# Performance work log

Hardware: AMD Instinct MI355X
Metric: run time of the kernel (lower is better)

Reference implementation:

```python
import jax, jax.numpy as jnp
import numpy as np

STRIDE, PADDING, DILATION, K = 1, 1, 1, 3


def setup_inputs() -> dict:
    key = jax.random.key(0)
    kx, kw, kb = jax.random.split(key, 3)
    x = jax.random.normal(kx, (8, 64, 56, 56), jnp.float32)
    weight = jax.random.normal(kw, (64, 64, K, K), jnp.float32) * 0.05
    bias = jax.random.normal(kb, (64,), jnp.float32)
    # 256x256 LUT of (approximate) int8 products; here the exact product table
    # q_i * q_j for q in [-128, 127], indexed by (q+128).
    q = jnp.arange(256, dtype=jnp.float32) - 128.0
    lut = q[:, None] * q[None, :]
    return {"x": x, "weight": weight, "bias": bias, "lut": lut}


def _quant_int8(t):
    # symmetric per-tensor int8 quantization
    s = jnp.max(jnp.abs(t)) / 127.0
    q = jnp.clip(jnp.round(t / s), -128.0, 127.0).astype(jnp.int32)
    return q, s


def _lut_conv(x, weight, lut):
    B, C, H, W = x.shape
    O = weight.shape[0]
    xq, sx = _quant_int8(x)
    wq, sw = _quant_int8(weight)
    # im2col: patches [B, C*K*K, Ho, Wo]; zero padding quantizes to index 128 (q=0)
    patches = jax.lax.conv_general_dilated_patches(
        xq.astype(jnp.float32), (K, K), (STRIDE, STRIDE),
        [(PADDING, PADDING), (PADDING, PADDING)],
        rhs_dilation=(DILATION, DILATION))
    _, CKK, Ho, Wo = patches.shape
    P = Ho * Wo
    xp = patches.astype(jnp.int32).reshape(B, CKK, P).transpose(0, 2, 1)  # [B,P,CKK]
    wq_flat = wq.reshape(O, CKK)                                          # [O,CKK]
    lut_flat = lut.reshape(-1)                                            # [65536]
    base = (xp + 128) * 256                                               # [B,P,CKK]

    def step(carry, w_o):
        # gather approximate products for one output channel and accumulate
        vals = jnp.take(lut_flat, base + (w_o + 128))  # [B,P,CKK]
        return carry, vals.sum(-1)                     # [B,P]

    _, acc = jax.lax.scan(step, None, wq_flat)         # [O,B,P]
    out = acc.transpose(1, 0, 2).reshape(B, O, Ho, Wo) * (sx * sw)
    return out


def reference(x, weight, bias, lut):
    return _lut_conv(x, weight, lut) + bias[None, :, None, None]
```

## Files before the change

kernel.cpp:

```cpp
#include <hip/hip_runtime.h>


#define BATCH 8
#define CIN   64
#define HH    56
#define WW    56
#define OUTC  64
#define IMG   (HH * WW)
#define TW    58

typedef unsigned int u32;
typedef int v4i __attribute__((ext_vector_type(4)));

__device__ __forceinline__ u32 qpack4(float v0, float v1, float v2, float v3, float s) {
    u32 p = 0;
    float q;
    q = fminf(fmaxf(rintf(v0 / s), -128.0f), 127.0f); p |= ((u32)((int)q & 0xff));
    q = fminf(fmaxf(rintf(v1 / s), -128.0f), 127.0f); p |= ((u32)((int)q & 0xff)) << 8;
    q = fminf(fmaxf(rintf(v2 / s), -128.0f), 127.0f); p |= ((u32)((int)q & 0xff)) << 16;
    q = fminf(fmaxf(rintf(v3 / s), -128.0f), 127.0f); p |= ((u32)((int)q & 0xff)) << 24;
    return p;
}

__global__ __launch_bounds__(256) void max_quantw_kernel(
    const float4* __restrict__ x4, const float4* __restrict__ w4,
    const float* __restrict__ wt,
    float* __restrict__ partsx, u32* __restrict__ wq,
    float* __restrict__ scales) {
    __shared__ float red[4];
    int t = threadIdx.x;
    int blk = blockIdx.x;
    if (blk < 784) {
        int base = blk * 512 + t;
        float4 a = x4[base];
        float4 b = x4[base + 256];
        float m = fmaxf(fmaxf(fmaxf(fabsf(a.x), fabsf(a.y)), fmaxf(fabsf(a.z), fabsf(a.w))),
                        fmaxf(fmaxf(fabsf(b.x), fabsf(b.y)), fmaxf(fabsf(b.z), fabsf(b.w))));
        #pragma unroll
        for (int off = 32; off > 0; off >>= 1)
            m = fmaxf(m, __shfl_down(m, off));
        if ((t & 63) == 0) red[t >> 6] = m;
        __syncthreads();
        if (t == 0)
            partsx[blk] = fmaxf(fmaxf(red[0], red[1]), fmaxf(red[2], red[3]));
    } else {
        float m = 0.0f;
        #pragma unroll 4
        for (int k = 0; k < 36; ++k) {
            float4 a = w4[k * 256 + t];
            m = fmaxf(m, fmaxf(fmaxf(fabsf(a.x), fabsf(a.y)), fmaxf(fabsf(a.z), fabsf(a.w))));
        }
        #pragma unroll
        for (int off = 32; off > 0; off >>= 1)
            m = fmaxf(m, __shfl_down(m, off));
        if ((t & 63) == 0) red[t >> 6] = m;
        __syncthreads();
        float mw = fmaxf(fmaxf(red[0], red[1]), fmaxf(red[2], red[3]));
        float sw = mw / 127.0f;
        if (blk == 784 && t == 0) scales[0] = sw;
        int oc = (blk - 784) * 16 + (t >> 4);
        int cg = t & 15;
        const float4* wb = (const float4*)(wt + oc * 576 + cg * 36);
        float v[36];
        #pragma unroll
        for (int i = 0; i < 9; ++i) {
            float4 f = wb[i];
            v[4 * i + 0] = f.x; v[4 * i + 1] = f.y;
            v[4 * i + 2] = f.z; v[4 * i + 3] = f.w;
        }
        #pragma unroll
        for (int tap = 0; tap < 9; ++tap)
            wq[(oc * 9 + tap) * 16 + cg] =
                qpack4(v[tap], v[9 + tap], v[18 + tap], v[27 + tap], sw);
    }
}

__global__ __launch_bounds__(256) void fused_conv_kernel(
    const float* __restrict__ x, const u32* __restrict__ wq,
    const float* __restrict__ partsx, const float* __restrict__ scales,
    const float* __restrict__ bias, float* __restrict__ out) {
    __shared__ char wl[576 * 80];
    __shared__ char xl[232 * 80];
    __shared__ float sred[4];

    int t = threadIdx.x;
    int lane = t & 63, wid = t >> 6;

    float m = fmaxf(fmaxf(partsx[t], partsx[t + 256]), partsx[t + 512]);
    if (t < 16) m = fmaxf(m, partsx[t + 768]);
    #pragma unroll
    for (int off = 32; off > 0; off >>= 1)
        m = fmaxf(m, __shfl_down(m, off));
    if (lane == 0) sred[wid] = m;
    __syncthreads();
    float mx = fmaxf(fmaxf(sred[0], sred[1]), fmaxf(sred[2], sred[3]));
    float sx = mx / 127.0f;
    float sw = scales[0];

    #pragma unroll
    for (int i = 0; i < 9; ++i) {
        int g = i * 256 + t;
        v4i v = *(const v4i*)((const char*)wq + (size_t)g * 16);
        *(v4i*)(wl + (g >> 2) * 80 + (g & 3) * 16) = v;
    }

    int p0 = blockIdx.x * 64;
    int b = p0 / IMG;
    int hw0 = p0 % IMG;
    int r0 = hw0 / WW;
    #pragma unroll
    for (int iter = 0; iter < 4; ++iter) {
        int item = iter * 256 + t;
        if (item < 928) {
            int s = item >> 2;
            int cg = item & 3;
            int i = s / TW, j2 = s % TW;
            int ro = r0 - 1 + i;
            int co = j2 - 1;
            u32 q0 = 0, q1 = 0, q2 = 0, q3 = 0;
            if (ro >= 0 && ro < HH && co >= 0 && co < WW) {
                const float* xb = x + ((size_t)(b * CIN + cg * 16)) * IMG + ro * WW + co;
                q0 = qpack4(xb[0 * IMG], xb[1 * IMG], xb[2 * IMG], xb[3 * IMG], sx);
                q1 = qpack4(xb[4 * IMG], xb[5 * IMG], xb[6 * IMG], xb[7 * IMG], sx);
                q2 = qpack4(xb[8 * IMG], xb[9 * IMG], xb[10 * IMG], xb[11 * IMG], sx);
                q3 = qpack4(xb[12 * IMG], xb[13 * IMG], xb[14 * IMG], xb[15 * IMG], sx);
            }
            v4i qv = {(int)q0, (int)q1, (int)q2, (int)q3};
            *(v4i*)(xl + s * 80 + cg * 16) = qv;
        }
    }
    __syncthreads();

    int m16 = lane & 15, kq = lane >> 4;
    int prel = wid * 16 + m16;
    int hw = hw0 + prel;
    int h = hw / WW, w = hw % WW;
    const char* abase = xl + ((h - r0) * TW + w) * 80 + kq * 16;
    const char* bbase = wl + m16 * 9 * 80 + kq * 16;

    v4i acc0 = {0, 0, 0, 0}, acc1 = {0, 0, 0, 0};
    v4i acc2 = {0, 0, 0, 0}, acc3 = {0, 0, 0, 0};
    #pragma unroll
    for (int kh = 0; kh < 3; ++kh) {
        #pragma unroll
        for (int kw = 0; kw < 3; ++kw) {
            int tap = kh * 3 + kw;
            v4i av = *(const v4i*)(abase + (kh * TW + kw) * 80);
            v4i b0 = *(const v4i*)(bbase + tap * 80);
            v4i b1 = *(const v4i*)(bbase + tap * 80 + 16 * 9 * 80);
            v4i b2 = *(const v4i*)(bbase + tap * 80 + 32 * 9 * 80);
            v4i b3 = *(const v4i*)(bbase + tap * 80 + 48 * 9 * 80);
            acc0 = __builtin_amdgcn_mfma_i32_16x16x64_i8(av, b0, acc0, 0, 0, 0);
            acc1 = __builtin_amdgcn_mfma_i32_16x16x64_i8(av, b1, acc1, 0, 0, 0);
            acc2 = __builtin_amdgcn_mfma_i32_16x16x64_i8(av, b2, acc2, 0, 0, 0);
            acc3 = __builtin_amdgcn_mfma_i32_16x16x64_i8(av, b3, acc3, 0, 0, 0);
        }
    }

    float scale = sx * sw;
    int pout = hw0 + wid * 16 + kq * 4;
    v4i accs[4] = {acc0, acc1, acc2, acc3};
    #pragma unroll
    for (int tile = 0; tile < 4; ++tile) {
        int oc = tile * 16 + m16;
        float bv = bias[oc];
        float4 r;
        r.x = (float)accs[tile][0] * scale + bv;
        r.y = (float)accs[tile][1] * scale + bv;
        r.z = (float)accs[tile][2] * scale + bv;
        r.w = (float)accs[tile][3] * scale + bv;
        *(float4*)(out + ((size_t)(b * OUTC + oc)) * IMG + pout) = r;
    }
}

extern "C" void kernel_launch(void* const* d_in, const int* in_sizes, int n_in,
                              void* d_out, int out_size, void* d_ws, size_t ws_size,
                              hipStream_t stream) {
    const float* x    = (const float*)d_in[0];
    const float* wt   = (const float*)d_in[1];
    const float* bias = (const float*)d_in[2];

    char* ws = (char*)d_ws;
    float* partsx = (float*)ws;
    float* scales = (float*)(ws + 3200);
    u32*   wq     = (u32*)(ws + 4096);

    max_quantw_kernel<<<788, 256, 0, stream>>>(
        (const float4*)x, (const float4*)wt, wt, partsx, wq, scales);
    fused_conv_kernel<<<392, 256, 0, stream>>>(
        x, wq, partsx, scales, bias, (float*)d_out);
}
```

Before: 85.19 us.

## Split activation quantization into separate kernel writing padded int8 NHWC buffer

Moves int8 quantization of x out of the conv kernel into a dedicated kernel that writes a zero-padded NHWC int8 tensor to workspace, with extra blocks writing the border zeros. The conv kernel then reads MFMA A operands directly from global memory instead of building a halo tile in LDS. This removes the redundant halo quantization, about 3.6x per pixel across 16-channel strided loads, and cuts the fp32 reads. The cost is an extra kernel launch, a global round trip of the int8 activations, and uncoalesced global A loads in the MFMA loop.

```diff
diff --git a/kernel.cpp b/kernel.cpp
--- a/kernel.cpp
+++ b/kernel.cpp
@@ -7,7 +7,8 @@
 #define WW    56
 #define OUTC  64
 #define IMG   (HH * WW)
-#define TW    58
+#define HP    58
+#define WP    58
 
 typedef unsigned int u32;
 typedef int v4i __attribute__((ext_vector_type(4)));
@@ -75,67 +76,86 @@
     }
 }
 
-__global__ __launch_bounds__(256) void fused_conv_kernel(
-    const float* __restrict__ x, const u32* __restrict__ wq,
-    const float* __restrict__ partsx, const float* __restrict__ scales,
-    const float* __restrict__ bias, float* __restrict__ out) {
-    __shared__ char wl[576 * 80];
-    __shared__ char xl[232 * 80];
+__global__ __launch_bounds__(256) void quant_kernel(
+    const float* __restrict__ x, const float* __restrict__ partsx,
+    u32* __restrict__ xq, float* __restrict__ scales) {
     __shared__ float sred[4];
-
+    __shared__ char xl[64 * 80];
     int t = threadIdx.x;
     int lane = t & 63, wid = t >> 6;
-
-    float m = fmaxf(fmaxf(partsx[t], partsx[t + 256]), partsx[t + 512]);
-    if (t < 16) m = fmaxf(m, partsx[t + 768]);
-    #pragma unroll
-    for (int off = 32; off > 0; off >>= 1)
-        m = fmaxf(m, __shfl_down(m, off));
-    if (lane == 0) sred[wid] = m;
-    __syncthreads();
-    float mx = fmaxf(fmaxf(sred[0], sred[1]), fmaxf(sred[2], sred[3]));
-    float sx = mx / 127.0f;
-    float sw = scales[0];
-
+    int blk = blockIdx.x;
+
+    if (blk < 392) {
+        float m = fmaxf(fmaxf(partsx[t], partsx[t + 256]), partsx[t + 512]);
+        if (t < 16) m = fmaxf(m, partsx[t + 768]);
+        #pragma unroll
+        for (int off = 32; off > 0; off >>= 1)
+            m = fmaxf(m, __shfl_down(m, off));
+        if (lane == 0) sred[wid] = m;
+        __syncthreads();
+        float mx = fmaxf(fmaxf(sred[0], sred[1]), fmaxf(sred[2], sred[3]));
+        float sx = mx / 127.0f;
+        if (blk == 0 && t == 0) scales[1] = sx;
+
+        int p0 = blk * 64;
+        int b = p0 / IMG;
+        int hw0 = p0 % IMG;
+        int pl = t & 63;
+        int cg = t >> 6;
+        int hw = hw0 + pl;
+        const float* xb = x + ((size_t)(b * CIN + cg * 16)) * IMG + hw;
+        #pragma unroll
+        for (int k = 0; k < 4; ++k) {
+            float v0 = xb[(4 * k + 0) * IMG];
+            float v1 = xb[(4 * k + 1) * IMG];
+            float v2 = xb[(4 * k + 2) * IMG];
+            float v3 = xb[(4 * k + 3) * IMG];
+            *(u32*)(xl + pl * 80 + cg * 16 + k * 4) = qpack4(v0, v1, v2, v3, sx);
+        }
+        __syncthreads();
+        v4i val = *(const v4i*)(xl + (t >> 2) * 80 + (t & 3) * 16);
+        int p = p0 + (t >> 2);
+        int hwp = p % IMG;
+        int h = hwp / WW, w = hwp % WW;
+        *(v4i*)((char*)xq + (((size_t)(b * HP + h + 1) * WP + (w + 1)) * 64) + (t & 3) * 16) = val;
+    } else {
+        int b = blk - 392;
+        v4i z = {0, 0, 0, 0};
+        for (int idx = t; idx < 912; idx += 256) {
+            int s = idx >> 2, chunk = idx & 3;
+            int hp, wp;
+            if (s < 58)       { hp = 0;  wp = s; }
+            else if (s < 116) { hp = 57; wp = s - 58; }
+            else { int s2 = s - 116; hp = 1 + (s2 >> 1); wp = (s2 & 1) * 57; }
+            *(v4i*)((char*)xq + (((size_t)(b * HP + hp) * WP + wp) * 64) + chunk * 16) = z;
+        }
+    }
+}
+
+__global__ __launch_bounds__(256) void conv_mfma_kernel(
+    const char* __restrict__ xqb, const u32* __restrict__ wq,
+    const float* __restrict__ scales, const float* __restrict__ bias,
+    float* __restrict__ out) {
+    __shared__ char wl[576 * 80];
+    int t = threadIdx.x;
     #pragma unroll
     for (int i = 0; i < 9; ++i) {
         int g = i * 256 + t;
         v4i v = *(const v4i*)((const char*)wq + (size_t)g * 16);
         *(v4i*)(wl + (g >> 2) * 80 + (g & 3) * 16) = v;
     }
+    __syncthreads();
+
+    int lane = t & 63, wid = t >> 6;
+    int m16 = lane & 15, kq = lane >> 4;
 
     int p0 = blockIdx.x * 64;
     int b = p0 / IMG;
     int hw0 = p0 % IMG;
-    int r0 = hw0 / WW;
-    #pragma unroll
-    for (int iter = 0; iter < 4; ++iter) {
-        int item = iter * 256 + t;
-        if (item < 928) {
-            int s = item >> 2;
-            int cg = item & 3;
-            int i = s / TW, j2 = s % TW;
-            int ro = r0 - 1 + i;
-            int co = j2 - 1;
-            u32 q0 = 0, q1 = 0, q2 = 0, q3 = 0;
-            if (ro >= 0 && ro < HH && co >= 0 && co < WW) {
-                const float* xb = x + ((size_t)(b * CIN + cg * 16)) * IMG + ro * WW + co;
-                q0 = qpack4(xb[0 * IMG], xb[1 * IMG], xb[2 * IMG], xb[3 * IMG], sx);
-                q1 = qpack4(xb[4 * IMG], xb[5 * IMG], xb[6 * IMG], xb[7 * IMG], sx);
-                q2 = qpack4(xb[8 * IMG], xb[9 * IMG], xb[10 * IMG], xb[11 * IMG], sx);
-                q3 = qpack4(xb[12 * IMG], xb[13 * IMG], xb[14 * IMG], xb[15 * IMG], sx);
-            }
-            v4i qv = {(int)q0, (int)q1, (int)q2, (int)q3};
-            *(v4i*)(xl + s * 80 + cg * 16) = qv;
-        }
-    }
-    __syncthreads();
-
-    int m16 = lane & 15, kq = lane >> 4;
-    int prel = wid * 16 + m16;
-    int hw = hw0 + prel;
+    int p = p0 + wid * 16 + m16;
+    int hw = p % IMG;
     int h = hw / WW, w = hw % WW;
-    const char* abase = xl + ((h - r0) * TW + w) * 80 + kq * 16;
+    const char* aptr = xqb + (((size_t)(b * HP + h) * WP + w) * 64 + kq * 16);
     const char* bbase = wl + m16 * 9 * 80 + kq * 16;
 
     v4i acc0 = {0, 0, 0, 0}, acc1 = {0, 0, 0, 0};
@@ -145,7 +165,7 @@
         #pragma unroll
         for (int kw = 0; kw < 3; ++kw) {
             int tap = kh * 3 + kw;
-            v4i av = *(const v4i*)(abase + (kh * TW + kw) * 80);
+            v4i av = *(const v4i*)(aptr + (kh * WP + kw) * 64);
             v4i b0 = *(const v4i*)(bbase + tap * 80);
             v4i b1 = *(const v4i*)(bbase + tap * 80 + 16 * 9 * 80);
             v4i b2 = *(const v4i*)(bbase + tap * 80 + 32 * 9 * 80);
@@ -157,7 +177,7 @@
         }
     }
 
-    float scale = sx * sw;
+    float scale = scales[0] * scales[1];
     int pout = hw0 + wid * 16 + kq * 4;
     v4i accs[4] = {acc0, acc1, acc2, acc3};
     #pragma unroll
@@ -184,9 +204,12 @@
     float* partsx = (float*)ws;
     float* scales = (float*)(ws + 3200);
     u32*   wq     = (u32*)(ws + 4096);
+    u32*   xq     = (u32*)(ws + 4096 + 36864);
 
     max_quantw_kernel<<<788, 256, 0, stream>>>(
         (const float4*)x, (const float4*)wt, wt, partsx, wq, scales);
-    fused_conv_kernel<<<392, 256, 0, stream>>>(
-        x, wq, partsx, scales, bias, (float*)d_out);
-}
+    quant_kernel<<<400, 256, 0, stream>>>(
+        x, partsx, xq, scales);
+    conv_mfma_kernel<<<392, 256, 0, stream>>>(
+        (const char*)xq, wq, scales, bias, (float*)d_out);
+}
```

Result: faster. 80.08 us (-6.0%).
